# Kernel optimization log

Measured on AMD Instinct MI355X. Metric: run time of the kernel, lower is better.

The kernel has to match this reference:

```python
import jax, jax.numpy as jnp
import numpy as np
from jax import lax

ROT_ANG = 2.0 * np.pi
EPS_FFT = 1e-15
EPS_NORM = 1e-12


def _bilinear_sample(img, px, py):
    # img: [B, C, H, W]; px, py: [n, n] pixel coords. Zero padding outside.
    H, W = img.shape[-2], img.shape[-1]
    x0 = jnp.floor(px)
    y0 = jnp.floor(py)
    wx1 = px - x0
    wy1 = py - y0
    wx0 = 1.0 - wx1
    wy0 = 1.0 - wy1

    def gather(yf, xf, w):
        valid = (yf >= 0) & (yf <= H - 1) & (xf >= 0) & (xf <= W - 1)
        yc = jnp.clip(yf, 0, H - 1).astype(jnp.int32)
        xc = jnp.clip(xf, 0, W - 1).astype(jnp.int32)
        vals = img[:, :, yc, xc]  # [B, C, n, n]
        return vals * (w * valid)[None, None]

    return (gather(y0, x0, wy0 * wx0) + gather(y0, x0 + 1, wy0 * wx1)
            + gather(y0 + 1, x0, wy1 * wx0) + gather(y0 + 1, x0 + 1, wy1 * wx1))


def _radon(img, angles):
    # Parallel-beam Radon: sinogram[b, c, a, s] = line integral along direction
    # (cos a, sin a) at detector offset s (bilinear interp, zero outside image).
    n = img.shape[-1]
    c = (n - 1) / 2.0
    grid = jnp.arange(n, dtype=jnp.float32) - c  # centered coords
    s = grid[:, None]  # detector offset  [n, 1]
    t = grid[None, :]  # along-ray coord  [1, n]

    def one_angle(_, theta):
        ct, st = jnp.cos(theta), jnp.sin(theta)
        px = c + s * ct - t * st  # [n, n]
        py = c + s * st + t * ct
        vals = _bilinear_sample(img, px, py)  # [B, C, n, n]
        return None, vals.sum(-1)  # integrate along ray -> [B, C, n]

    _, sino = lax.scan(one_angle, None, angles)  # [A, B, C, n]
    return jnp.moveaxis(sino, 0, 2)  # [B, C, A, n]


def _forward(bev):
    B = bev.shape[0]
    n_angles = bev.shape[-2]
    angles = jnp.asarray(np.linspace(0.0, ROT_ANG, n_angles).astype(np.float32))
    sinogram = _radon(bev, angles)  # [B, C, A, n]
    # forward_row_fft: 1D FFT along last dim (ortho), magnitude with eps
    f = jnp.fft.fft(sinogram, axis=-1, norm='ortho')
    spec = jnp.sqrt(jnp.real(f) ** 2 + jnp.imag(f) ** 2 + EPS_FFT)
    x = spec.sum(axis=-2).reshape(B, -1)  # sum over angle dim -> [B, C*n]
    # F.normalize(x, dim=-1)
    x = x / jnp.maximum(jnp.linalg.norm(x, axis=-1, keepdims=True), EPS_NORM)
    return x


def setup_inputs() -> dict:
    key = jax.random.key(0)
    bev = jax.random.uniform(key, (1024, 1, 120, 120), dtype=jnp.float32)
    return {"bev": bev}


def reference(bev):
    return _forward(bev)
```

## Files before the change

kernel.cpp:

```cpp
#include <hip/hip_runtime.h>
#include <hip/hip_fp16.h>
#include <math.h>

#define NPIX  120
#define NS    120
#define NK    61
#define HSTR  123
#define HROWS 123
#define CHUNK 8
#define NCHUNK 15
#define NT    960

#if __has_builtin(__builtin_amdgcn_fractf)
#define FRACTF(x) __builtin_amdgcn_fractf(x)
#else
#define FRACTF(x) ((x) - floorf(x))
#endif


__global__ void ring_fused(const float* __restrict__ bev,
                           float* __restrict__ out,
                           int B) {
    __shared__ __half2 H[HROWS * HSTR];
    __shared__ float2 schunk[CHUNK * NS];
    __shared__ float2 outAcc[NK];
    __shared__ float invN[2];

    const int tid = threadIdx.x;
    const int b0  = blockIdx.x * 2;
    const int b1  = b0 + 1;
    const int al  = tid / NS;
    const int sk  = tid - al * NS;
    if (b0 >= B) return;

    const float* srcA = bev + (size_t)b0 * (NPIX * NPIX);
    const float* srcB = (b1 < B) ? bev + (size_t)b1 * (NPIX * NPIX) : srcA;
    for (int i = tid; i < HROWS * HSTR; i += NT) {
        int y = i / HSTR, x = i - y * HSTR;
        float va = 0.f, vb = 0.f;
        int gx = x - 1, gy = y - 1;
        if (gx >= 0 && gx < NPIX && gy >= 0 && gy < NPIX) {
            va = srcA[gy * NPIX + gx];
            vb = srcB[gy * NPIX + gx];
        }
        H[i] = __floats2half2_rn(va, vb);
    }
    __syncthreads();

    const float coef = 2.f * cosf((float)sk * 0.052359877559829887f);
    const float sgn  = (sk & 1) ? -1.f : 1.f;
    const double STEP = 6.283185307179586 / 119.0;
    float accKA = 0.f, accKB = 0.f;

    for (int ch = 0; ch < NCHUNK; ++ch) {
        {
            int a = ch * CHUNK + al;
            float theta = (float)((double)a * STEP);
            float st = sinf(theta), ct = cosf(theta);
            float sf  = (float)sk - 59.5f;
            float Ax  = fmaf(sf, ct, 60.5f);
            float Ay  = fmaf(sf, st, 60.5f);
            float nst = -st;
            float aA0 = 0.f, aA1 = 0.f;
            float aB0 = 0.f, aB1 = 0.f;
            float tv  = -59.5f;
            #pragma unroll 4
            for (int t = 0; t < NPIX; ++t) {
                float px = fmaf(tv, nst, Ax);
                float py = fmaf(tv, ct,  Ay);
                float cx = fminf(fmaxf(px, 0.f), 121.5f);
                float cy = fminf(fmaxf(py, 0.f), 121.5f);
                int   ix = (int)cx;
                int   iy = (int)cy;
                float wx = FRACTF(cx);
                float wy = FRACTF(cy);
                int   ai = __mul24(iy, HSTR) + ix;
                __half2 c00 = H[ai];
                __half2 c01 = H[ai + 1];
                __half2 c10 = H[ai + HSTR];
                __half2 c11 = H[ai + HSTR + 1];
                __half2 wx2 = __float2half2_rn(wx);
                __half2 wy2 = __float2half2_rn(wy);
                __half2 th  = __hfma2(wx2, __hsub2(c01, c00), c00);
                __half2 bh  = __hfma2(wx2, __hsub2(c11, c10), c10);
                __half2 vh  = __hfma2(wy2, __hsub2(bh, th), th);
                if (t & 1) { aA1 += __low2float(vh); aB1 += __high2float(vh); }
                else       { aA0 += __low2float(vh); aB0 += __high2float(vh); }
                tv += 1.f;
            }
            schunk[al * NS + sk] = make_float2(aA0 + aA1, aB0 + aB1);
        }
        __syncthreads();

        if (sk < NK) {
            const float2* row = schunk + al * NS;
            float u1a = 0.f, u2a = 0.f, u1b = 0.f, u2b = 0.f;
            #pragma unroll 4
            for (int s = 0; s < 60; ++s) {
                float2 lo = row[s];
                float2 hi = row[s + 60];
                float wa = fmaf(sgn, hi.x, lo.x);
                float wb = fmaf(sgn, hi.y, lo.y);
                float va = fmaf(coef, u1a, wa - u2a); u2a = u1a; u1a = va;
                float vb = fmaf(coef, u1b, wb - u2b); u2b = u1b; u1b = vb;
            }
            float pa = fmaf(u1a, u1a, fmaf(u2a, u2a, -coef * u1a * u2a));
            float pb = fmaf(u1b, u1b, fmaf(u2b, u2b, -coef * u1b * u2b));
            pa = fmaxf(pa, 0.f);
            pb = fmaxf(pb, 0.f);
            accKA += sqrtf(fmaf(pa, (1.f / 120.f), 1e-15f));
            accKB += sqrtf(fmaf(pb, (1.f / 120.f), 1e-15f));
        }
        __syncthreads();
    }

    if (sk < NK) schunk[al * NS + sk] = make_float2(accKA, accKB);
    __syncthreads();
    if (tid < NK) {
        float sa = 0.f, sb = 0.f;
        for (int a2 = 0; a2 < CHUNK; ++a2) {
            float2 v = schunk[a2 * NS + tid];
            sa += v.x;
            sb += v.y;
        }
        outAcc[tid] = make_float2(sa, sb);
    }
    __syncthreads();

    if (tid < 2) {
        float ssq = 0.f;
        for (int k = 0; k < NK; ++k) {
            float2 oa = outAcc[k];
            float v = tid ? oa.y : oa.x;
            float wgt = (k == 0 || k == 60) ? 1.f : 2.f;
            ssq = fmaf(wgt * v, v, ssq);
        }
        invN[tid] = 1.f / fmaxf(sqrtf(ssq), 1e-12f);
    }
    __syncthreads();

    if (tid < 2 * NPIX) {
        int img = tid / NPIX;
        int j   = tid - img * NPIX;
        int k   = (j <= 60) ? j : (NPIX - j);
        int bb  = b0 + img;
        if (bb < B) {
            float2 oa = outAcc[k];
            float v = (img ? oa.y : oa.x) * invN[img];
            out[(size_t)bb * NPIX + j] = v;
        }
    }
}

extern "C" void kernel_launch(void* const* d_in, const int* in_sizes, int n_in,
                              void* d_out, int out_size, void* d_ws, size_t ws_size,
                              hipStream_t stream) {
    const float* bev = (const float*)d_in[0];
    float* out = (float*)d_out;
    int B = in_sizes[0] / (NPIX * NPIX);
    int grid = (B + 1) / 2;
    hipLaunchKernelGGL(ring_fused, dim3(grid), dim3(NT), 0, stream, bev, out, B);
}
```

Baseline: 690.9 us.

## Process four images per block with packed half2 pairs and double-buffered chunks

```diff
diff --git a/kernel.cpp b/kernel.cpp
--- a/kernel.cpp
+++ b/kernel.cpp
@@ -17,42 +17,49 @@
 #define FRACTF(x) ((x) - floorf(x))
 #endif
 
+__device__ __forceinline__ __half2 lo_h2(uint2 q) { return *reinterpret_cast<__half2*>(&q.x); }
+__device__ __forceinline__ __half2 hi_h2(uint2 q) { return *reinterpret_cast<__half2*>(&q.y); }
 
 __global__ void ring_fused(const float* __restrict__ bev,
                            float* __restrict__ out,
                            int B) {
-    __shared__ __half2 H[HROWS * HSTR];
-    __shared__ float2 schunk[CHUNK * NS];
-    __shared__ float2 outAcc[NK];
-    __shared__ float invN[2];
+    __shared__ uint2  H[HROWS * HSTR];
+    __shared__ float4 schunk[2][CHUNK * NS];
+    __shared__ float4 outAcc[NK];
+    __shared__ float  invN[4];
 
     const int tid = threadIdx.x;
-    const int b0  = blockIdx.x * 2;
-    const int b1  = b0 + 1;
+    const int b0  = blockIdx.x * 4;
     const int al  = tid / NS;
     const int sk  = tid - al * NS;
     if (b0 >= B) return;
 
-    const float* srcA = bev + (size_t)b0 * (NPIX * NPIX);
-    const float* srcB = (b1 < B) ? bev + (size_t)b1 * (NPIX * NPIX) : srcA;
+    const float* s0 = bev + (size_t)b0 * (NPIX * NPIX);
+    const float* s1 = (b0 + 1 < B) ? bev + (size_t)(b0 + 1) * (NPIX * NPIX) : s0;
+    const float* s2 = (b0 + 2 < B) ? bev + (size_t)(b0 + 2) * (NPIX * NPIX) : s0;
+    const float* s3 = (b0 + 3 < B) ? bev + (size_t)(b0 + 3) * (NPIX * NPIX) : s0;
     for (int i = tid; i < HROWS * HSTR; i += NT) {
         int y = i / HSTR, x = i - y * HSTR;
-        float va = 0.f, vb = 0.f;
+        float va = 0.f, vb = 0.f, vc = 0.f, vd = 0.f;
         int gx = x - 1, gy = y - 1;
         if (gx >= 0 && gx < NPIX && gy >= 0 && gy < NPIX) {
-            va = srcA[gy * NPIX + gx];
-            vb = srcB[gy * NPIX + gx];
+            int o = gy * NPIX + gx;
+            va = s0[o]; vb = s1[o]; vc = s2[o]; vd = s3[o];
         }
-        H[i] = __floats2half2_rn(va, vb);
+        __half2 ab = __floats2half2_rn(va, vb);
+        __half2 cd = __floats2half2_rn(vc, vd);
+        H[i] = make_uint2(*reinterpret_cast<unsigned*>(&ab),
+                          *reinterpret_cast<unsigned*>(&cd));
     }
     __syncthreads();
 
     const float coef = 2.f * cosf((float)sk * 0.052359877559829887f);
     const float sgn  = (sk & 1) ? -1.f : 1.f;
     const double STEP = 6.283185307179586 / 119.0;
-    float accKA = 0.f, accKB = 0.f;
+    float acc0 = 0.f, acc1 = 0.f, acc2 = 0.f, acc3 = 0.f;
 
     for (int ch = 0; ch < NCHUNK; ++ch) {
+        float4* buf = schunk[ch & 1];
         {
             int a = ch * CHUNK + al;
             float theta = (float)((double)a * STEP);
@@ -61,8 +68,8 @@
             float Ax  = fmaf(sf, ct, 60.5f);
             float Ay  = fmaf(sf, st, 60.5f);
             float nst = -st;
-            float aA0 = 0.f, aA1 = 0.f;
-            float aB0 = 0.f, aB1 = 0.f;
+            float aA0 = 0.f, aA1 = 0.f, aB0 = 0.f, aB1 = 0.f;
+            float aC0 = 0.f, aC1 = 0.f, aD0 = 0.f, aD1 = 0.f;
             float tv  = -59.5f;
             #pragma unroll 4
             for (int t = 0; t < NPIX; ++t) {
@@ -75,63 +82,79 @@
                 float wx = FRACTF(cx);
                 float wy = FRACTF(cy);
                 int   ai = __mul24(iy, HSTR) + ix;
-                __half2 c00 = H[ai];
-                __half2 c01 = H[ai + 1];
-                __half2 c10 = H[ai + HSTR];
-                __half2 c11 = H[ai + HSTR + 1];
+                uint2 q00 = H[ai];
+                uint2 q01 = H[ai + 1];
+                uint2 q10 = H[ai + HSTR];
+                uint2 q11 = H[ai + HSTR + 1];
                 __half2 wx2 = __float2half2_rn(wx);
                 __half2 wy2 = __float2half2_rn(wy);
-                __half2 th  = __hfma2(wx2, __hsub2(c01, c00), c00);
-                __half2 bh  = __hfma2(wx2, __hsub2(c11, c10), c10);
-                __half2 vh  = __hfma2(wy2, __hsub2(bh, th), th);
-                if (t & 1) { aA1 += __low2float(vh); aB1 += __high2float(vh); }
-                else       { aA0 += __low2float(vh); aB0 += __high2float(vh); }
+                __half2 abT = __hfma2(wx2, __hsub2(lo_h2(q01), lo_h2(q00)), lo_h2(q00));
+                __half2 abB = __hfma2(wx2, __hsub2(lo_h2(q11), lo_h2(q10)), lo_h2(q10));
+                __half2 abV = __hfma2(wy2, __hsub2(abB, abT), abT);
+                __half2 cdT = __hfma2(wx2, __hsub2(hi_h2(q01), hi_h2(q00)), hi_h2(q00));
+                __half2 cdB = __hfma2(wx2, __hsub2(hi_h2(q11), hi_h2(q10)), hi_h2(q10));
+                __half2 cdV = __hfma2(wy2, __hsub2(cdB, cdT), cdT);
+                if (t & 1) {
+                    aA1 += __low2float(abV); aB1 += __high2float(abV);
+                    aC1 += __low2float(cdV); aD1 += __high2float(cdV);
+                } else {
+                    aA0 += __low2float(abV); aB0 += __high2float(abV);
+                    aC0 += __low2float(cdV); aD0 += __high2float(cdV);
+                }
                 tv += 1.f;
             }
-            schunk[al * NS + sk] = make_float2(aA0 + aA1, aB0 + aB1);
+            buf[al * NS + sk] = make_float4(aA0 + aA1, aB0 + aB1,
+                                            aC0 + aC1, aD0 + aD1);
         }
         __syncthreads();
 
         if (sk < NK) {
-            const float2* row = schunk + al * NS;
+            const float4* row = buf + al * NS;
             float u1a = 0.f, u2a = 0.f, u1b = 0.f, u2b = 0.f;
+            float u1c = 0.f, u2c = 0.f, u1d = 0.f, u2d = 0.f;
             #pragma unroll 4
             for (int s = 0; s < 60; ++s) {
-                float2 lo = row[s];
-                float2 hi = row[s + 60];
+                float4 lo = row[s];
+                float4 hi = row[s + 60];
                 float wa = fmaf(sgn, hi.x, lo.x);
                 float wb = fmaf(sgn, hi.y, lo.y);
+                float wc = fmaf(sgn, hi.z, lo.z);
+                float wd = fmaf(sgn, hi.w, lo.w);
                 float va = fmaf(coef, u1a, wa - u2a); u2a = u1a; u1a = va;
                 float vb = fmaf(coef, u1b, wb - u2b); u2b = u1b; u1b = vb;
+                float vc = fmaf(coef, u1c, wc - u2c); u2c = u1c; u1c = vc;
+                float vd = fmaf(coef, u1d, wd - u2d); u2d = u1d; u1d = vd;
             }
             float pa = fmaf(u1a, u1a, fmaf(u2a, u2a, -coef * u1a * u2a));
             float pb = fmaf(u1b, u1b, fmaf(u2b, u2b, -coef * u1b * u2b));
-            pa = fmaxf(pa, 0.f);
-            pb = fmaxf(pb, 0.f);
-            accKA += sqrtf(fmaf(pa, (1.f / 120.f), 1e-15f));
-            accKB += sqrtf(fmaf(pb, (1.f / 120.f), 1e-15f));
+            float pc = fmaf(u1c, u1c, fmaf(u2c, u2c, -coef * u1c * u2c));
+            float pd = fmaf(u1d, u1d, fmaf(u2d, u2d, -coef * u1d * u2d));
+            pa = fmaxf(pa, 0.f); pb = fmaxf(pb, 0.f);
+            pc = fmaxf(pc, 0.f); pd = fmaxf(pd, 0.f);
+            acc0 += sqrtf(fmaf(pa, (1.f / 120.f), 1e-15f));
+            acc1 += sqrtf(fmaf(pb, (1.f / 120.f), 1e-15f));
+            acc2 += sqrtf(fmaf(pc, (1.f / 120.f), 1e-15f));
+            acc3 += sqrtf(fmaf(pd, (1.f / 120.f), 1e-15f));
         }
-        __syncthreads();
-    }
-
-    if (sk < NK) schunk[al * NS + sk] = make_float2(accKA, accKB);
-    __syncthreads();
-    if (tid < NK) {
-        float sa = 0.f, sb = 0.f;
-        for (int a2 = 0; a2 < CHUNK; ++a2) {
-            float2 v = schunk[a2 * NS + tid];
-            sa += v.x;
-            sb += v.y;
-        }
-        outAcc[tid] = make_float2(sa, sb);
     }
     __syncthreads();
 
-    if (tid < 2) {
+    if (sk < NK) schunk[0][al * NS + sk] = make_float4(acc0, acc1, acc2, acc3);
+    __syncthreads();
+    if (tid < NK) {
+        float sa = 0.f, sb = 0.f, sc = 0.f, sd = 0.f;
+        for (int a2 = 0; a2 < CHUNK; ++a2) {
+            float4 v = schunk[0][a2 * NS + tid];
+            sa += v.x; sb += v.y; sc += v.z; sd += v.w;
+        }
+        outAcc[tid] = make_float4(sa, sb, sc, sd);
+    }
+    __syncthreads();
+
+    if (tid < 4) {
         float ssq = 0.f;
         for (int k = 0; k < NK; ++k) {
-            float2 oa = outAcc[k];
-            float v = tid ? oa.y : oa.x;
+            float v = ((const float*)&outAcc[k])[tid];
             float wgt = (k == 0 || k == 60) ? 1.f : 2.f;
             ssq = fmaf(wgt * v, v, ssq);
         }
@@ -139,14 +162,13 @@
     }
     __syncthreads();
 
-    if (tid < 2 * NPIX) {
+    if (tid < 4 * NPIX) {
         int img = tid / NPIX;
         int j   = tid - img * NPIX;
         int k   = (j <= 60) ? j : (NPIX - j);
         int bb  = b0 + img;
         if (bb < B) {
-            float2 oa = outAcc[k];
-            float v = (img ? oa.y : oa.x) * invN[img];
+            float v = ((const float*)&outAcc[k])[img] * invN[img];
             out[(size_t)bb * NPIX + j] = v;
         }
     }
@@ -158,6 +180,6 @@
     const float* bev = (const float*)d_in[0];
     float* out = (float*)d_out;
     int B = in_sizes[0] / (NPIX * NPIX);
-    int grid = (B + 1) / 2;
+    int grid = (B + 3) / 4;
     hipLaunchKernelGGL(ring_fused, dim3(grid), dim3(NT), 0, stream, bev, out, B);
 }
```

After: 600.5 us. 1.15x faster.
